# Kernel optimization log

Measured on AMD Instinct MI355X. Metric: run time of the kernel, lower is better.

The kernel has to match this reference:

```python
import jax, jax.numpy as jnp
import numpy as np

B, L, D, H = 2, 256, 256, 4
DH = D // H  # 64


def setup_inputs() -> dict:
    key = jax.random.key(0)
    ks = jax.random.split(key, 20)
    inp = {
        "q": jax.random.normal(ks[0], (B, L, D), jnp.float32),
        "k": jax.random.normal(ks[1], (B, L, D), jnp.float32),
        "v": jax.random.normal(ks[2], (B, L, D), jnp.float32),
        "attn_mask": jnp.zeros((L, L), jnp.float32),  # nonzero => masked
        "key_padding_mask": jnp.zeros((B, L), bool),
        "pitch_rel": jax.random.normal(ks[3], (B, L, L, D), jnp.float32),
        "dur_rel": jax.random.normal(ks[4], (B, L, L, D), jnp.float32),
    }
    scale = 1.0 / np.sqrt(D)
    names = ["Wq", "Wk", "Wv", "fc", "pr", "dr"]
    for i, n in enumerate(names):
        inp[n + "_w"] = jax.random.normal(ks[5 + 2 * i], (D, D), jnp.float32) * scale
        inp[n + "_b"] = jax.random.normal(ks[6 + 2 * i], (D,), jnp.float32) * 0.01
    return inp


def _linear(x, w, b):
    # torch nn.Linear: y = x @ W^T + b
    return jnp.matmul(x, w.T) + b


def reference(q, k, v, attn_mask, key_padding_mask, pitch_rel, dur_rel,
              Wq_w, Wq_b, Wk_w, Wk_b, Wv_w, Wv_b, fc_w, fc_b,
              pr_w, pr_b, dr_w, dr_b):
    Bq, Lq, Dm = q.shape
    Lk = k.shape[1]
    # project and split heads -> (B, H, L, DH)
    def heads(x, w, b):
        return _linear(x, w, b).reshape(Bq, -1, H, DH).transpose(0, 2, 1, 3)
    qh, kh, vh = heads(q, Wq_w, Wq_b), heads(k, Wk_w, Wk_b), heads(v, Wv_w, Wv_b)

    # content scores: (B, H, Lq, Lk)
    logits = jnp.einsum("bhid,bhjd->bhij", qh, kh)

    # relative pitch bias: pitch_rel (B, Lq, Lk, D) -> (B, Lq, Lk, H, DH)
    pr = _linear(pitch_rel, pr_w, pr_b).reshape(Bq, Lq, Lk, H, DH)
    logits = logits + jnp.einsum("bhid,bijhd->bhij", qh, pr)

    dr = _linear(dur_rel, dr_w, dr_b).reshape(Bq, Lq, Lk, H, DH)
    logits = logits + jnp.einsum("bhid,bijhd->bhij", qh, dr)

    logits = logits / np.sqrt(DH)

    # mask: key_padding_mask broadcast over the QUERY axis (as in source),
    # attn_mask nonzero => masked
    mask = jnp.logical_or(key_padding_mask[:, None, :, None],
                          (attn_mask != 0)[None, None, :, :])
    logits = jnp.where(mask, jnp.float32(-9e15), logits)

    attn = jax.nn.softmax(logits, axis=-1)  # (B, H, Lq, Lk)
    out = jnp.einsum("bhij,bhjd->bhid", attn, vh)  # (B, H, Lq, DH)
    out = out.transpose(0, 2, 1, 3).reshape(Bq, Lq, Dm)
    out = _linear(out, fc_w, fc_b)  # dropout is identity in eval mode
    return out, attn
```

## Files before the change

kernel.cpp:

```cpp
#include <hip/hip_runtime.h>
#include <math.h>


typedef float nfloat4 __attribute__((ext_vector_type(4)));

static __device__ __forceinline__ float4 ntload4(const float4* p) {
  nfloat4 r = __builtin_nontemporal_load((const nfloat4*)p);
  return make_float4(r.x, r.y, r.z, r.w);
}

__global__ __launch_bounds__(256) void k_transpose(const float* __restrict__ in,
                                                   float* __restrict__ out) {
  __shared__ float t[32][33];
  int bx = blockIdx.x & 7, by = blockIdx.x >> 3;
  int x = threadIdx.x & 31, y0 = threadIdx.x >> 5;
#pragma unroll
  for (int yy = 0; yy < 32; yy += 8)
    t[yy + y0][x] = in[(size_t)(by * 32 + yy + y0) * 256 + bx * 32 + x];
  __syncthreads();
#pragma unroll
  for (int yy = 0; yy < 32; yy += 8)
    out[(size_t)(bx * 32 + yy + y0) * 256 + by * 32 + x] = t[x][yy + y0];
}

__global__ __launch_bounds__(256) void k_proj(
    const float* __restrict__ q, const float* __restrict__ k_, const float* __restrict__ v,
    const float* __restrict__ Wq, const float* __restrict__ Bq,
    const float* __restrict__ Wk, const float* __restrict__ Bk,
    const float* __restrict__ Wv, const float* __restrict__ Bv,
    float* __restrict__ qh, float* __restrict__ kh, float* __restrict__ vh) {
  int blk = blockIdx.x;
  int m = blk >> 5;
  int r = blk & 31;
  int b = r >> 4, it = (r >> 2) & 3, ot = r & 3;
  const float* X = (m == 0) ? q : (m == 1) ? k_ : v;
  const float* W = (m == 0) ? Wq : (m == 1) ? Wk : Wv;
  const float* Bs = (m == 0) ? Bq : (m == 1) ? Bk : Bv;
  float* OUT = (m == 0) ? qh : (m == 1) ? kh : vh;
  const float scale = (m == 0) ? 0.125f : 1.0f;

  __shared__ float xs[64][33];
  __shared__ float ws[64][33];
  int tid = threadIdx.x;
  int ti = tid >> 4, to = tid & 15;
  int lr = tid >> 2, lc = (tid & 3) * 8;
  float acc[4][4] = {};

  for (int k0 = 0; k0 < 256; k0 += 32) {
    float4 a0 = *(const float4*)(X + (size_t)(b * 256 + it * 64 + lr) * 256 + k0 + lc);
    float4 a1 = *(const float4*)(X + (size_t)(b * 256 + it * 64 + lr) * 256 + k0 + lc + 4);
    xs[lr][lc + 0] = a0.x; xs[lr][lc + 1] = a0.y; xs[lr][lc + 2] = a0.z; xs[lr][lc + 3] = a0.w;
    xs[lr][lc + 4] = a1.x; xs[lr][lc + 5] = a1.y; xs[lr][lc + 6] = a1.z; xs[lr][lc + 7] = a1.w;
    float4 w0 = *(const float4*)(W + (size_t)(ot * 64 + lr) * 256 + k0 + lc);
    float4 w1 = *(const float4*)(W + (size_t)(ot * 64 + lr) * 256 + k0 + lc + 4);
    ws[lr][lc + 0] = w0.x; ws[lr][lc + 1] = w0.y; ws[lr][lc + 2] = w0.z; ws[lr][lc + 3] = w0.w;
    ws[lr][lc + 4] = w1.x; ws[lr][lc + 5] = w1.y; ws[lr][lc + 6] = w1.z; ws[lr][lc + 7] = w1.w;
    __syncthreads();
#pragma unroll
    for (int kk = 0; kk < 32; ++kk) {
      float xv0 = xs[ti * 4 + 0][kk], xv1 = xs[ti * 4 + 1][kk];
      float xv2 = xs[ti * 4 + 2][kk], xv3 = xs[ti * 4 + 3][kk];
      float wv0 = ws[0 * 16 + to][kk], wv1 = ws[1 * 16 + to][kk];
      float wv2 = ws[2 * 16 + to][kk], wv3 = ws[3 * 16 + to][kk];
      acc[0][0] += xv0 * wv0; acc[0][1] += xv0 * wv1; acc[0][2] += xv0 * wv2; acc[0][3] += xv0 * wv3;
      acc[1][0] += xv1 * wv0; acc[1][1] += xv1 * wv1; acc[1][2] += xv1 * wv2; acc[1][3] += xv1 * wv3;
      acc[2][0] += xv2 * wv0; acc[2][1] += xv2 * wv1; acc[2][2] += xv2 * wv2; acc[2][3] += xv2 * wv3;
      acc[3][0] += xv3 * wv0; acc[3][1] += xv3 * wv1; acc[3][2] += xv3 * wv2; acc[3][3] += xv3 * wv3;
    }
    __syncthreads();
  }
#pragma unroll
  for (int ii = 0; ii < 4; ++ii)
#pragma unroll
    for (int oo = 0; oo < 4; ++oo) {
      int i = it * 64 + ti * 4 + ii;
      int dd = oo * 16 + to;
      OUT[(size_t)((b * 4 + ot) * 256 + i) * 64 + dd] = (acc[ii][oo] + Bs[ot * 64 + dd]) * scale;
    }
}

__global__ __launch_bounds__(256) void k_qprdr(
    const float* __restrict__ qh, const float* __restrict__ prw,
    const float* __restrict__ drw, float* __restrict__ qpr, float* __restrict__ qdr) {
  int blk = blockIdx.x;
  int t = blk >> 7;
  int r2 = blk & 127;
  int rt = r2 >> 2, et = r2 & 3;
  const float* W = t ? drw : prw;
  float* OUT = t ? qdr : qpr;
  int h = (rt >> 2) & 3;

  __shared__ float xs[64][33];
  __shared__ float ws2[32][64];
  int tid = threadIdx.x;
  int ti = tid >> 4, to = tid & 15;
  float acc[4][4] = {};

  for (int k0 = 0; k0 < 64; k0 += 32) {
    int lr = tid >> 2, lc = (tid & 3) * 8;
    float4 a0 = *(const float4*)(qh + (size_t)(rt * 64 + lr) * 64 + k0 + lc);
    float4 a1 = *(const float4*)(qh + (size_t)(rt * 64 + lr) * 64 + k0 + lc + 4);
    xs[lr][lc + 0] = a0.x; xs[lr][lc + 1] = a0.y; xs[lr][lc + 2] = a0.z; xs[lr][lc + 3] = a0.w;
    xs[lr][lc + 4] = a1.x; xs[lr][lc + 5] = a1.y; xs[lr][lc + 6] = a1.z; xs[lr][lc + 7] = a1.w;
    int wr = tid >> 3, wc = (tid & 7) * 8;
    float4 w0 = *(const float4*)(W + (size_t)(h * 64 + k0 + wr) * 256 + et * 64 + wc);
    float4 w1 = *(const float4*)(W + (size_t)(h * 64 + k0 + wr) * 256 + et * 64 + wc + 4);
    ws2[wr][wc + 0] = w0.x; ws2[wr][wc + 1] = w0.y; ws2[wr][wc + 2] = w0.z; ws2[wr][wc + 3] = w0.w;
    ws2[wr][wc + 4] = w1.x; ws2[wr][wc + 5] = w1.y; ws2[wr][wc + 6] = w1.z; ws2[wr][wc + 7] = w1.w;
    __syncthreads();
#pragma unroll
    for (int kk = 0; kk < 32; ++kk) {
      float xv0 = xs[ti * 4 + 0][kk], xv1 = xs[ti * 4 + 1][kk];
      float xv2 = xs[ti * 4 + 2][kk], xv3 = xs[ti * 4 + 3][kk];
      float wv0 = ws2[kk][0 * 16 + to], wv1 = ws2[kk][1 * 16 + to];
      float wv2 = ws2[kk][2 * 16 + to], wv3 = ws2[kk][3 * 16 + to];
      acc[0][0] += xv0 * wv0; acc[0][1] += xv0 * wv1; acc[0][2] += xv0 * wv2; acc[0][3] += xv0 * wv3;
      acc[1][0] += xv1 * wv0; acc[1][1] += xv1 * wv1; acc[1][2] += xv1 * wv2; acc[1][3] += xv1 * wv3;
      acc[2][0] += xv2 * wv0; acc[2][1] += xv2 * wv1; acc[2][2] += xv2 * wv2; acc[2][3] += xv2 * wv3;
      acc[3][0] += xv3 * wv0; acc[3][1] += xv3 * wv1; acc[3][2] += xv3 * wv2; acc[3][3] += xv3 * wv3;
    }
    __syncthreads();
  }
#pragma unroll
  for (int ii = 0; ii < 4; ++ii)
#pragma unroll
    for (int oo = 0; oo < 4; ++oo)
      OUT[(size_t)(rt * 64 + ti * 4 + ii) * 256 + et * 64 + oo * 16 + to] = acc[ii][oo];
}

__global__ __launch_bounds__(256) void k_qk(const float* __restrict__ qh,
                                            const float* __restrict__ kh,
                                            float* __restrict__ qk) {
  int blk = blockIdx.x;
  int bh = blk >> 4, it = (blk >> 2) & 3, jt = blk & 3;
  __shared__ float xs[64][33];
  __shared__ float ys[64][33];
  int tid = threadIdx.x;
  int ti = tid >> 4, to = tid & 15;
  float acc[4][4] = {};

  for (int k0 = 0; k0 < 64; k0 += 32) {
    int lr = tid >> 2, lc = (tid & 3) * 8;
    float4 a0 = *(const float4*)(qh + (size_t)(bh * 256 + it * 64 + lr) * 64 + k0 + lc);
    float4 a1 = *(const float4*)(qh + (size_t)(bh * 256 + it * 64 + lr) * 64 + k0 + lc + 4);
    xs[lr][lc + 0] = a0.x; xs[lr][lc + 1] = a0.y; xs[lr][lc + 2] = a0.z; xs[lr][lc + 3] = a0.w;
    xs[lr][lc + 4] = a1.x; xs[lr][lc + 5] = a1.y; xs[lr][lc + 6] = a1.z; xs[lr][lc + 7] = a1.w;
    float4 b0 = *(const float4*)(kh + (size_t)(bh * 256 + jt * 64 + lr) * 64 + k0 + lc);
    float4 b1 = *(const float4*)(kh + (size_t)(bh * 256 + jt * 64 + lr) * 64 + k0 + lc + 4);
    ys[lr][lc + 0] = b0.x; ys[lr][lc + 1] = b0.y; ys[lr][lc + 2] = b0.z; ys[lr][lc + 3] = b0.w;
    ys[lr][lc + 4] = b1.x; ys[lr][lc + 5] = b1.y; ys[lr][lc + 6] = b1.z; ys[lr][lc + 7] = b1.w;
    __syncthreads();
#pragma unroll
    for (int kk = 0; kk < 32; ++kk) {
      float xv0 = xs[ti * 4 + 0][kk], xv1 = xs[ti * 4 + 1][kk];
      float xv2 = xs[ti * 4 + 2][kk], xv3 = xs[ti * 4 + 3][kk];
      float wv0 = ys[0 * 16 + to][kk], wv1 = ys[1 * 16 + to][kk];
      float wv2 = ys[2 * 16 + to][kk], wv3 = ys[3 * 16 + to][kk];
      acc[0][0] += xv0 * wv0; acc[0][1] += xv0 * wv1; acc[0][2] += xv0 * wv2; acc[0][3] += xv0 * wv3;
      acc[1][0] += xv1 * wv0; acc[1][1] += xv1 * wv1; acc[1][2] += xv1 * wv2; acc[1][3] += xv1 * wv3;
      acc[2][0] += xv2 * wv0; acc[2][1] += xv2 * wv1; acc[2][2] += xv2 * wv2; acc[2][3] += xv2 * wv3;
      acc[3][0] += xv3 * wv0; acc[3][1] += xv3 * wv1; acc[3][2] += xv3 * wv2; acc[3][3] += xv3 * wv3;
    }
    __syncthreads();
  }
#pragma unroll
  for (int ii = 0; ii < 4; ++ii)
#pragma unroll
    for (int jj = 0; jj < 4; ++jj)
      qk[(size_t)(bh * 256 + it * 64 + ti * 4 + ii) * 256 + jt * 64 + jj * 16 + to] = acc[ii][jj];
}

__global__ __launch_bounds__(256, 2) void k_fused(
    const float* __restrict__ pitch, const float* __restrict__ dur,
    const float* __restrict__ qpr, const float* __restrict__ qdr,
    const float* __restrict__ amask, const unsigned char* __restrict__ kpm,
    const float* __restrict__ vh, const float* __restrict__ fcT,
    const float* __restrict__ fcb, float* __restrict__ attn,
    float* __restrict__ out) {
  int bi = blockIdx.x;
  int b = bi >> 8, i = bi & 255;
  int tid = threadIdx.x, w = tid >> 6, l = tid & 63;
  int jbase = w * 64;

  __shared__ float red[4][8][4][65];
  __shared__ float logits[4][264];
  __shared__ float pre[256];

  float4 qp[4], qd[4];
#pragma unroll
  for (int h = 0; h < 4; ++h) {
    qp[h] = *(const float4*)(qpr + (size_t)((b * 4 + h) * 256 + i) * 256 + 4 * l);
    qd[h] = *(const float4*)(qdr + (size_t)((b * 4 + h) * 256 + i) * 256 + 4 * l);
  }

  int p = l & 31;
  int jj_o = p >> 2, h_o = p & 3;
  size_t qrow0 = (size_t)((b * 4 + h_o) * 256 + i) * 256 + jbase + jj_o;
  bool rowm = kpm[b * 256 + i] != 0;
  float qk8[8];
  int mbits = 0;
#pragma unroll
  for (int g = 0; g < 8; ++g) {
    qk8[g] = attn[qrow0 + 8 * g];
    if (rowm || amask[(size_t)i * 256 + jbase + g * 8 + jj_o] != 0.f) mbits |= (1 << g);
  }

  const float4* prow =
      (const float4*)(pitch + (size_t)(b * 256 + i) * 65536) + (size_t)jbase * 64 + l;
  const float4* drow =
      (const float4*)(dur + (size_t)(b * 256 + i) * 65536) + (size_t)jbase * 64 + l;

  float4 Pa[8], Da[8], Pb[8], Db[8];

#define LOADG(PB, DB, g)                                  \
  {                                                       \
    _Pragma("unroll") for (int t = 0; t < 8; ++t) {       \
      PB[t] = ntload4(prow + ((g) * 8 + t) * 64);         \
      DB[t] = ntload4(drow + ((g) * 8 + t) * 64);         \
    }                                                     \
  }

#define CSTORE(PB, DB, g)                                                       \
  {                                                                             \
    _Pragma("unroll") for (int t = 0; t < 8; ++t) {                             \
      _Pragma("unroll") for (int h = 0; h < 4; ++h) {                           \
        red[w][t][h][l] =                                                       \
            PB[t].x * qp[h].x + PB[t].y * qp[h].y + PB[t].z * qp[h].z +         \
            PB[t].w * qp[h].w + DB[t].x * qd[h].x + DB[t].y * qd[h].y +         \
            DB[t].z * qd[h].z + DB[t].w * qd[h].w;                              \
      }                                                                         \
    }                                                                           \
    float x = 0.f;                                                              \
    {                                                                           \
      const float* rr = &red[w][jj_o][h_o][(l >> 5) * 32];                      \
      _Pragma("unroll 8") for (int c = 0; c < 32; ++c) x += rr[c];              \
    }                                                                           \
    x += __shfl_xor(x, 32);                                                     \
    if (l < 32) {                                                               \
      float val = qk8[g] + x;                                                   \
      if (mbits & (1 << (g))) val = -9e15f;                                     \
      logits[h_o][jbase + (g) * 8 + jj_o] = val;                                \
    }                                                                           \
  }

  LOADG(Pa, Da, 0);
#pragma unroll
  for (int gg = 0; gg < 4; ++gg) {
    LOADG(Pb, Db, 2 * gg + 1);
    CSTORE(Pa, Da, 2 * gg);
    if (gg < 3) LOADG(Pa, Da, 2 * gg + 2);
    CSTORE(Pb, Db, 2 * gg + 1);
  }
#undef LOADG
#undef CSTORE
  __syncthreads();

  float* lrow = &logits[w][0];
  float4 v4 = *(float4*)(lrow + 4 * l);
  float mx = fmaxf(fmaxf(v4.x, v4.y), fmaxf(v4.z, v4.w));
#pragma unroll
  for (int m = 1; m <= 32; m <<= 1) mx = fmaxf(mx, __shfl_xor(mx, m));
  float e0 = __expf(v4.x - mx), e1 = __expf(v4.y - mx);
  float e2 = __expf(v4.z - mx), e3 = __expf(v4.w - mx);
  float sm = e0 + e1 + e2 + e3;
#pragma unroll
  for (int m = 1; m <= 32; m <<= 1) sm += __shfl_xor(sm, m);
  float inv = 1.0f / sm;
  float4 a4 = make_float4(e0 * inv, e1 * inv, e2 * inv, e3 * inv);
  *(float4*)(lrow + 4 * l) = a4;
  *(float4*)(attn + (size_t)((b * 4 + w) * 256 + i) * 256 + 4 * l) = a4;
  __syncthreads();

  float acc = 0.f;
  const float* vbase = vh + (size_t)(b * 4 + w) * 256 * 64 + l;
#pragma unroll 4
  for (int jj = 0; jj < 256; ++jj) acc += lrow[jj] * vbase[(size_t)jj * 64];
  pre[tid] = acc;
  __syncthreads();

  float acc2 = fcb[tid];
#pragma unroll 4
  for (int c = 0; c < 256; ++c) acc2 += pre[c] * fcT[(size_t)c * 256 + tid];
  out[(size_t)(b * 256 + i) * 256 + tid] = acc2;
}

extern "C" void kernel_launch(void* const* d_in, const int* in_sizes, int n_in,
                              void* d_out, int out_size, void* d_ws, size_t ws_size,
                              hipStream_t stream) {
  (void)in_sizes; (void)n_in; (void)out_size; (void)ws_size;
  const float* q = (const float*)d_in[0];
  const float* k = (const float*)d_in[1];
  const float* v = (const float*)d_in[2];
  const float* amask = (const float*)d_in[3];
  const unsigned char* kpm = (const unsigned char*)d_in[4];
  const float* pitch = (const float*)d_in[5];
  const float* dur = (const float*)d_in[6];
  const float* Wq = (const float*)d_in[7];
  const float* Bq = (const float*)d_in[8];
  const float* Wk = (const float*)d_in[9];
  const float* Bk = (const float*)d_in[10];
  const float* Wv = (const float*)d_in[11];
  const float* Bv = (const float*)d_in[12];
  const float* fcw = (const float*)d_in[13];
  const float* fcb = (const float*)d_in[14];
  const float* prw = (const float*)d_in[15];
  const float* drw = (const float*)d_in[17];

  float* out = (float*)d_out;
  float* attn = out + 2 * 256 * 256;

  float* wsf = (float*)d_ws;
  float* qh = wsf;
  float* kh = qh + 131072;
  float* vh = kh + 131072;
  float* qpr = vh + 131072;
  float* qdr = qpr + 524288;
  float* fcT = qdr + 524288;

  k_transpose<<<64, 256, 0, stream>>>(fcw, fcT);
  k_proj<<<96, 256, 0, stream>>>(q, k, v, Wq, Bq, Wk, Bk, Wv, Bv, qh, kh, vh);
  k_qprdr<<<256, 256, 0, stream>>>(qh, prw, drw, qpr, qdr);
  k_qk<<<128, 256, 0, stream>>>(qh, kh, attn);
  k_fused<<<512, 256, 0, stream>>>(pitch, dur, qpr, qdr, amask, kpm, vh, fcT, fcb, attn, out);
}
```

Before: 116.6 us.

## Stream pitch/dur rows via async global-to-LDS loads and merge middle kernels

The main fused kernel now stages pitch and duration rows into shared memory through global_load_lds, using a four-deep ring buffer and explicit vmcnt waits. Before, it used a register double buffer of nontemporal loads. Reductions are regrouped into batches of four rows. The goal is to hide HBM latency for the dominant pitch/dur stream without register pressure. The transpose, qprdr and qk kernels are merged into one launch to cut launch overhead. The 128KB of staging shared memory limits occupancy to one block per CU (launch_bounds changed to 1), which may reduce latency hiding between blocks.

```diff
diff --git a/kernel.cpp b/kernel.cpp
--- a/kernel.cpp
+++ b/kernel.cpp
@@ -2,25 +2,14 @@
 #include <math.h>
 
 
-typedef float nfloat4 __attribute__((ext_vector_type(4)));
-
-static __device__ __forceinline__ float4 ntload4(const float4* p) {
-  nfloat4 r = __builtin_nontemporal_load((const nfloat4*)p);
-  return make_float4(r.x, r.y, r.z, r.w);
-}
-
-__global__ __launch_bounds__(256) void k_transpose(const float* __restrict__ in,
-                                                   float* __restrict__ out) {
-  __shared__ float t[32][33];
-  int bx = blockIdx.x & 7, by = blockIdx.x >> 3;
-  int x = threadIdx.x & 31, y0 = threadIdx.x >> 5;
-#pragma unroll
-  for (int yy = 0; yy < 32; yy += 8)
-    t[yy + y0][x] = in[(size_t)(by * 32 + yy + y0) * 256 + bx * 32 + x];
-  __syncthreads();
-#pragma unroll
-  for (int yy = 0; yy < 32; yy += 8)
-    out[(size_t)(bx * 32 + yy + y0) * 256 + by * 32 + x] = t[x][yy + y0];
+template <int N> static __device__ __forceinline__ void vwait() {
+  asm volatile("s_waitcnt vmcnt(%0)" ::"i"(N) : "memory");
+}
+
+static __device__ __forceinline__ void gld16(const float* g, float* l) {
+  __builtin_amdgcn_global_load_lds(
+      (const __attribute__((address_space(1))) unsigned int*)g,
+      (__attribute__((address_space(3))) unsigned int*)l, 16, 0, 0);
 }
 
 __global__ __launch_bounds__(256) void k_proj(
@@ -79,10 +68,9 @@
     }
 }
 
-__global__ __launch_bounds__(256) void k_qprdr(
-    const float* __restrict__ qh, const float* __restrict__ prw,
-    const float* __restrict__ drw, float* __restrict__ qpr, float* __restrict__ qdr) {
-  int blk = blockIdx.x;
+static __device__ void body_qprdr(int blk, const float* __restrict__ qh,
+                                  const float* __restrict__ prw, const float* __restrict__ drw,
+                                  float* __restrict__ qpr, float* __restrict__ qdr) {
   int t = blk >> 7;
   int r2 = blk & 127;
   int rt = r2 >> 2, et = r2 & 3;
@@ -128,10 +116,8 @@
       OUT[(size_t)(rt * 64 + ti * 4 + ii) * 256 + et * 64 + oo * 16 + to] = acc[ii][oo];
 }
 
-__global__ __launch_bounds__(256) void k_qk(const float* __restrict__ qh,
-                                            const float* __restrict__ kh,
-                                            float* __restrict__ qk) {
-  int blk = blockIdx.x;
+static __device__ void body_qk(int blk, const float* __restrict__ qh,
+                               const float* __restrict__ kh, float* __restrict__ qk) {
   int bh = blk >> 4, it = (blk >> 2) & 3, jt = blk & 3;
   __shared__ float xs[64][33];
   __shared__ float ys[64][33];
@@ -170,7 +156,32 @@
       qk[(size_t)(bh * 256 + it * 64 + ti * 4 + ii) * 256 + jt * 64 + jj * 16 + to] = acc[ii][jj];
 }
 
-__global__ __launch_bounds__(256, 2) void k_fused(
+static __device__ void body_transpose(int blk, const float* __restrict__ in,
+                                      float* __restrict__ out) {
+  __shared__ float t[32][33];
+  int bx = blk & 7, by = blk >> 3;
+  int x = threadIdx.x & 31, y0 = threadIdx.x >> 5;
+#pragma unroll
+  for (int yy = 0; yy < 32; yy += 8)
+    t[yy + y0][x] = in[(size_t)(by * 32 + yy + y0) * 256 + bx * 32 + x];
+  __syncthreads();
+#pragma unroll
+  for (int yy = 0; yy < 32; yy += 8)
+    out[(size_t)(bx * 32 + yy + y0) * 256 + by * 32 + x] = t[x][yy + y0];
+}
+
+__global__ __launch_bounds__(256) void k_mid(
+    const float* __restrict__ qh, const float* __restrict__ kh,
+    const float* __restrict__ prw, const float* __restrict__ drw,
+    float* __restrict__ qpr, float* __restrict__ qdr, float* __restrict__ qk,
+    const float* __restrict__ fcw, float* __restrict__ fcT) {
+  int blk = blockIdx.x;
+  if (blk < 256) body_qprdr(blk, qh, prw, drw, qpr, qdr);
+  else if (blk < 384) body_qk(blk - 256, qh, kh, qk);
+  else body_transpose(blk - 384, fcw, fcT);
+}
+
+__global__ __launch_bounds__(256, 1) void k_fused(
     const float* __restrict__ pitch, const float* __restrict__ dur,
     const float* __restrict__ qpr, const float* __restrict__ qdr,
     const float* __restrict__ amask, const unsigned char* __restrict__ kpm,
@@ -182,7 +193,8 @@
   int tid = threadIdx.x, w = tid >> 6, l = tid & 63;
   int jbase = w * 64;
 
-  __shared__ float red[4][8][4][65];
+  __shared__ float stg[4][4][2048];
+  __shared__ float red[4][4][4][65];
   __shared__ float logits[4][264];
   __shared__ float pre[256];
 
@@ -193,66 +205,74 @@
     qd[h] = *(const float4*)(qdr + (size_t)((b * 4 + h) * 256 + i) * 256 + 4 * l);
   }
 
-  int p = l & 31;
-  int jj_o = p >> 2, h_o = p & 3;
-  size_t qrow0 = (size_t)((b * 4 + h_o) * 256 + i) * 256 + jbase + jj_o;
+  int p2 = l & 15, row_o = p2 >> 2, h_o = p2 & 3, sub = l >> 4;
   bool rowm = kpm[b * 256 + i] != 0;
-  float qk8[8];
-  int mbits = 0;
-#pragma unroll
-  for (int g = 0; g < 8; ++g) {
-    qk8[g] = attn[qrow0 + 8 * g];
-    if (rowm || amask[(size_t)i * 256 + jbase + g * 8 + jj_o] != 0.f) mbits |= (1 << g);
-  }
-
-  const float4* prow =
-      (const float4*)(pitch + (size_t)(b * 256 + i) * 65536) + (size_t)jbase * 64 + l;
-  const float4* drow =
-      (const float4*)(dur + (size_t)(b * 256 + i) * 65536) + (size_t)jbase * 64 + l;
-
-  float4 Pa[8], Da[8], Pb[8], Db[8];
-
-#define LOADG(PB, DB, g)                                  \
-  {                                                       \
-    _Pragma("unroll") for (int t = 0; t < 8; ++t) {       \
-      PB[t] = ntload4(prow + ((g) * 8 + t) * 64);         \
-      DB[t] = ntload4(drow + ((g) * 8 + t) * 64);         \
-    }                                                     \
-  }
-
-#define CSTORE(PB, DB, g)                                                       \
-  {                                                                             \
-    _Pragma("unroll") for (int t = 0; t < 8; ++t) {                             \
-      _Pragma("unroll") for (int h = 0; h < 4; ++h) {                           \
-        red[w][t][h][l] =                                                       \
-            PB[t].x * qp[h].x + PB[t].y * qp[h].y + PB[t].z * qp[h].z +         \
-            PB[t].w * qp[h].w + DB[t].x * qd[h].x + DB[t].y * qd[h].y +         \
-            DB[t].z * qd[h].z + DB[t].w * qd[h].w;                              \
-      }                                                                         \
-    }                                                                           \
-    float x = 0.f;                                                              \
-    {                                                                           \
-      const float* rr = &red[w][jj_o][h_o][(l >> 5) * 32];                      \
-      _Pragma("unroll 8") for (int c = 0; c < 32; ++c) x += rr[c];              \
-    }                                                                           \
-    x += __shfl_xor(x, 32);                                                     \
-    if (l < 32) {                                                               \
-      float val = qk8[g] + x;                                                   \
-      if (mbits & (1 << (g))) val = -9e15f;                                     \
-      logits[h_o][jbase + (g) * 8 + jj_o] = val;                                \
-    }                                                                           \
-  }
-
-  LOADG(Pa, Da, 0);
-#pragma unroll
-  for (int gg = 0; gg < 4; ++gg) {
-    LOADG(Pb, Db, 2 * gg + 1);
-    CSTORE(Pa, Da, 2 * gg);
-    if (gg < 3) LOADG(Pa, Da, 2 * gg + 2);
-    CSTORE(Pb, Db, 2 * gg + 1);
-  }
-#undef LOADG
-#undef CSTORE
+  size_t qbase = (size_t)((b * 4 + h_o) * 256 + i) * 256 + jbase + row_o;
+  float qk_pre[16];
+  unsigned mb = 0;
+#pragma unroll
+  for (int g = 0; g < 16; ++g) {
+    qk_pre[g] = attn[qbase + 4 * g];
+    if (rowm || amask[(size_t)i * 256 + jbase + 4 * g + row_o] != 0.f) mb |= (1u << g);
+  }
+
+  const float* prow0 = pitch + ((size_t)(b * 256 + i) * 256 + jbase) * 256;
+  const float* drow0 = dur + ((size_t)(b * 256 + i) * 256 + jbase) * 256;
+
+  asm volatile("s_waitcnt vmcnt(0)" ::: "memory");
+
+#define STAGE(s, gs)                                                    \
+  {                                                                     \
+    _Pragma("unroll") for (int r = 0; r < 4; ++r) {                     \
+      gld16(prow0 + ((gs)*4 + r) * 256 + 4 * l, &stg[w][s][r * 256]);   \
+      gld16(drow0 + ((gs)*4 + r) * 256 + 4 * l, &stg[w][s][1024 + r * 256]); \
+    }                                                                   \
+  }
+
+#define COMPUTE(s, g)                                                   \
+  {                                                                     \
+    float ar[4][4];                                                     \
+    _Pragma("unroll") for (int r = 0; r < 4; ++r) {                     \
+      float4 P = *(const float4*)&stg[w][s][r * 256 + 4 * l];           \
+      float4 Dv = *(const float4*)&stg[w][s][1024 + r * 256 + 4 * l];   \
+      _Pragma("unroll") for (int h = 0; h < 4; ++h)                     \
+        ar[r][h] = P.x * qp[h].x + P.y * qp[h].y + P.z * qp[h].z +      \
+                   P.w * qp[h].w + Dv.x * qd[h].x + Dv.y * qd[h].y +    \
+                   Dv.z * qd[h].z + Dv.w * qd[h].w;                     \
+    }                                                                   \
+    _Pragma("unroll") for (int r = 0; r < 4; ++r)                       \
+      _Pragma("unroll") for (int h = 0; h < 4; ++h)                     \
+        red[w][r][h][l] = ar[r][h];                                     \
+    float x = 0.f;                                                      \
+    {                                                                   \
+      const float* rr = &red[w][row_o][h_o][sub * 16];                  \
+      _Pragma("unroll") for (int c = 0; c < 16; ++c) x += rr[c];        \
+    }                                                                   \
+    x += __shfl_xor(x, 16);                                             \
+    x += __shfl_xor(x, 32);                                             \
+    if (l < 16) {                                                       \
+      float val = qk_pre[g] + x;                                        \
+      if (mb & (1u << (g))) val = -9e15f;                               \
+      logits[h_o][jbase + (g)*4 + row_o] = val;                         \
+    }                                                                   \
+  }
+
+#define ITER(g, N)                                   \
+  {                                                  \
+    if ((g) + 3 < 16) STAGE((((g) + 3) & 3), (g) + 3); \
+    vwait<N>();                                      \
+    __builtin_amdgcn_sched_barrier(0);               \
+    COMPUTE(((g)&3), g);                             \
+  }
+
+  STAGE(0, 0); STAGE(1, 1); STAGE(2, 2);
+  ITER(0, 24)  ITER(1, 24)  ITER(2, 24)  ITER(3, 24)
+  ITER(4, 24)  ITER(5, 24)  ITER(6, 24)  ITER(7, 24)
+  ITER(8, 24)  ITER(9, 24)  ITER(10, 24) ITER(11, 24)
+  ITER(12, 24) ITER(13, 16) ITER(14, 8)  ITER(15, 0)
+#undef STAGE
+#undef COMPUTE
+#undef ITER
   __syncthreads();
 
   float* lrow = &logits[w][0];
@@ -317,9 +337,7 @@
   float* qdr = qpr + 524288;
   float* fcT = qdr + 524288;
 
-  k_transpose<<<64, 256, 0, stream>>>(fcw, fcT);
   k_proj<<<96, 256, 0, stream>>>(q, k, v, Wq, Bq, Wk, Bk, Wv, Bv, qh, kh, vh);
-  k_qprdr<<<256, 256, 0, stream>>>(qh, prw, drw, qpr, qdr);
-  k_qk<<<128, 256, 0, stream>>>(qh, kh, attn);
+  k_mid<<<448, 256, 0, stream>>>(qh, kh, prw, drw, qpr, qdr, attn, fcw, fcT);
   k_fused<<<512, 256, 0, stream>>>(pitch, dur, qpr, qdr, amask, kpm, vh, fcT, fcb, attn, out);
 }
```

New measurement: 139.1 us. +19.3%, slower.
